# Kernel tuning notes

Measured on AMD Instinct MI355X. Metric: run time of the kernel, lower is better.

The kernel has to match this reference:

```python
import jax, jax.numpy as jnp
import numpy as np

B, C, H, W = 8, 384, 32, 32
NUM_HEADS = 8
HEAD_DIM = C // NUM_HEADS
HIDDEN = max(32, C // 2)


def setup_inputs() -> dict:
    key = jax.random.key(0)
    ks = jax.random.split(key, 6)
    s = lambda fan_in: 1.0 / np.sqrt(fan_in)
    return {
        "x": jax.random.normal(ks[0], (B, C, H, W), dtype=jnp.float32),
        "qkv_w": jax.random.normal(ks[1], (C, 3 * C), dtype=jnp.float32) * s(C),
        "qkv_b": jnp.zeros((3 * C,), dtype=jnp.float32),
        "proj_w": jax.random.normal(ks[2], (C, C), dtype=jnp.float32) * s(C),
        "proj_b": jnp.zeros((C,), dtype=jnp.float32),
        "mlp_w1": jax.random.normal(ks[3], (2, HIDDEN), dtype=jnp.float32) * s(2),
        "mlp_b1": jnp.zeros((HIDDEN,), dtype=jnp.float32),
        "mlp_w2": jax.random.normal(ks[4], (HIDDEN, NUM_HEADS), dtype=jnp.float32) * s(HIDDEN),
        "mlp_b2": jnp.zeros((NUM_HEADS,), dtype=jnp.float32),
    }


def _relative_bias(h, w, mlp_w1, mlp_b1, mlp_w2, mlp_b2):
    ch = jnp.arange(h, dtype=jnp.float32)
    cw = jnp.arange(w, dtype=jnp.float32)
    coords = jnp.stack(jnp.meshgrid(ch, cw, indexing="ij"), axis=-1).reshape(-1, 2)  # [N,2]
    rel = coords[:, None, :] - coords[None, :, :]  # [N,N,2]
    denom = jnp.array([max(h - 1, 1), max(w - 1, 1)], dtype=jnp.float32)
    rel = rel / denom
    hidden = jax.nn.gelu(rel @ mlp_w1 + mlp_b1, approximate=False)
    bias = hidden @ mlp_w2 + mlp_b2  # [N,N,heads]
    return jnp.transpose(bias, (2, 0, 1))  # [heads,N,N]


def reference(x, qkv_w, qkv_b, proj_w, proj_b, mlp_w1, mlp_b1, mlp_w2, mlp_b2):
    b, c, h, w = x.shape
    n = h * w
    tokens = x.reshape(b, c, n).transpose(0, 2, 1)  # [B,N,C]
    qkv = (tokens @ qkv_w + qkv_b).reshape(b, n, 3, NUM_HEADS, HEAD_DIM)
    qkv = jnp.transpose(qkv, (2, 0, 3, 1, 4))  # [3,B,h,N,d]
    q, k, v = qkv[0], qkv[1], qkv[2]
    scale = HEAD_DIM ** -0.5
    attn = jnp.einsum("bhnd,bhmd->bhnm", q * scale, k)
    attn = attn + _relative_bias(h, w, mlp_w1, mlp_b1, mlp_w2, mlp_b2)[None]
    attn = jax.nn.softmax(attn, axis=-1)
    out = jnp.einsum("bhnm,bhmd->bhnd", attn, v)
    out = out.transpose(0, 2, 1, 3).reshape(b, n, c)
    out = out @ proj_w + proj_b
    return out.transpose(0, 2, 1).reshape(b, c, h, w)
```

## Files before the change

kernel.cpp:

```cpp
#include <hip/hip_runtime.h>
#include <hip/hip_bf16.h>
#include <math.h>

#define BB 8
#define CC 384
#define NT 1024
#define NHEAD 8
#define HD 48
#define HIDDEN 192
#define THREEC 1152

typedef short short8 __attribute__((ext_vector_type(8)));
typedef short short4v __attribute__((ext_vector_type(4)));
typedef float f32x4 __attribute__((ext_vector_type(4)));
typedef unsigned int uint2v __attribute__((ext_vector_type(2)));
typedef unsigned int uint4v __attribute__((ext_vector_type(4)));

static __device__ __forceinline__ short bf16bits(float v) {
  __hip_bfloat16 h = __float2bfloat16(v);
  return *(short*)&h;
}
static __device__ __forceinline__ unsigned cvtpk(float lo, float hi) {
  unsigned r;
  asm("v_cvt_pk_bf16_f32 %0, %1, %2" : "=v"(r) : "v"(lo), "v"(hi));
  return r;
}
static __device__ __forceinline__ void lds_dma16(const void* g, void* l) {
  __builtin_amdgcn_global_load_lds((const __attribute__((address_space(1))) unsigned*)g,
                                   (__attribute__((address_space(3))) unsigned*)l, 16, 0, 0);
}
static __device__ __forceinline__ void pl16swap(unsigned& a, unsigned& b) {
  asm("v_permlane16_swap_b32 %0, %1" : "+v"(a), "+v"(b));
}
static __device__ __forceinline__ float exp2_raw(float x) {
  float r;
  asm("v_exp_f32 %0, %1" : "=v"(r) : "v"(x));
  return r;
}

__global__ __launch_bounds__(256) void k_prep(
    const float* __restrict__ x, const float* __restrict__ qkv_w,
    const float* __restrict__ proj_w,
    const float* __restrict__ w1, const float* __restrict__ b1,
    const float* __restrict__ w2, const float* __restrict__ b2,
    __hip_bfloat16* __restrict__ xt, __hip_bfloat16* __restrict__ wtq,
    __hip_bfloat16* __restrict__ wtp, float* __restrict__ tab) {
  const int bid = blockIdx.x;
  const int tid = threadIdx.x;
  if (bid >= 3648) {
    int g = (bid - 3648) * 256 + tid;
    int p = g >> 3, jc = g & 7;
    if (p >= 63 * 63) return;
    float rh = (float)(p / 63 - 31) * (1.0f / 31.0f);
    float rw = (float)(p % 63 - 31) * (1.0f / 31.0f);
    float acc[8] = {0.f, 0.f, 0.f, 0.f, 0.f, 0.f, 0.f, 0.f};
    const int j0 = jc * 24;
#pragma unroll 4
    for (int j = j0; j < j0 + 24; j++) {
      float pre = fmaf(rh, w1[j], fmaf(rw, w1[HIDDEN + j], b1[j]));
      float gl = 0.5f * pre * (1.0f + erff(pre * 0.70710678118654752f));
#pragma unroll
      for (int h = 0; h < 8; h++) acc[h] = fmaf(gl, w2[j * 8 + h], acc[h]);
    }
#pragma unroll
    for (int msk = 1; msk <= 4; msk <<= 1)
#pragma unroll
      for (int h = 0; h < 8; h++) acc[h] += __shfl_xor(acc[h], msk);
    if (jc == 0) {
#pragma unroll
      for (int h = 0; h < 8; h++)
        tab[h * 3969 + p] = (acc[h] + b2[h]) * 1.4426950408889634f;
    }
    return;
  }
  const float* src;
  __hip_bfloat16* dst;
  int R, C, r0, c0;
  if (bid < 3072) {
    int zi = bid / 384, rem = bid % 384;
    R = 384; C = 1024;
    r0 = (rem / 32) * 32; c0 = (rem % 32) * 32;
    src = x + (size_t)zi * R * C;
    dst = xt + (size_t)zi * R * C;
  } else if (bid < 3504) {
    int i = bid - 3072;
    R = 384; C = 1152;
    r0 = (i / 36) * 32; c0 = (i % 36) * 32;
    src = qkv_w; dst = wtq;
  } else {
    int i = bid - 3504;
    R = 384; C = 384;
    r0 = (i / 12) * 32; c0 = (i % 12) * 32;
    src = proj_w; dst = wtp;
  }
  __shared__ float t[32][33];
#pragma unroll
  for (int e = 0; e < 4; e++) {
    int i = tid + e * 256;
    int r = i >> 5, c = i & 31;
    t[r][c] = src[(size_t)(r0 + r) * C + c0 + c];
  }
  __syncthreads();
#pragma unroll
  for (int e = 0; e < 4; e++) {
    int i = tid + e * 256;
    int c = i >> 5, r = i & 31;
    dst[(size_t)(c0 + c) * R + r0 + r] = __float2bfloat16(t[r][c]);
  }
}

__global__ __launch_bounds__(256) void k_qkv_mfma(
    const __hip_bfloat16* __restrict__ xt,
    const __hip_bfloat16* __restrict__ wtq,
    const float* __restrict__ qkv_b,
    __hip_bfloat16* __restrict__ Qb,
    __hip_bfloat16* __restrict__ Kb,
    __hip_bfloat16* __restrict__ Vt)
{
  __shared__ __align__(16) char smem[17408];
  short* As = (short*)smem;
  short* Bs = (short*)(smem + 8192);
  float* Vf = (float*)smem;
  const int n0 = blockIdx.x * 64;
  const int m0 = blockIdx.y * 64;
  const int tid = threadIdx.x;
  const int wv = tid >> 6, lane = tid & 63, quad = lane >> 4, lq = lane & 15;
  const int lrow = lane >> 3;
  const int gsw = ((lane & 7) ^ lrow) * 8;
  const int sw0 = (quad ^ (lq & 7)) * 8;
  const int sw1 = sw0 ^ 32;
  f32x4 acc[4];
#pragma unroll
  for (int nt = 0; nt < 4; nt++) acc[nt] = (f32x4){0.f, 0.f, 0.f, 0.f};
  for (int kk = 0; kk < CC; kk += 64) {
    __syncthreads();
    for (int c = wv; c < 16; c += 4) {
      if (c < 8)
        lds_dma16((const short*)xt + (size_t)(m0 + c * 8 + lrow) * 384 + kk + gsw,
                  smem + c * 1024);
      else
        lds_dma16((const short*)wtq + (size_t)(n0 + (c - 8) * 8 + lrow) * 384 + kk + gsw,
                  smem + 8192 + (c - 8) * 1024);
    }
    __syncthreads();
    short8 a0 = *(const short8*)(As + (wv * 16 + lq) * 64 + sw0);
    short8 a1 = *(const short8*)(As + (wv * 16 + lq) * 64 + sw1);
#pragma unroll
    for (int nt = 0; nt < 4; nt++) {
      acc[nt] = __builtin_amdgcn_mfma_f32_16x16x32_bf16(
          a0, *(const short8*)(Bs + (nt * 16 + lq) * 64 + sw0), acc[nt], 0, 0, 0);
      acc[nt] = __builtin_amdgcn_mfma_f32_16x16x32_bf16(
          a1, *(const short8*)(Bs + (nt * 16 + lq) * 64 + sw1), acc[nt], 0, 0, 0);
    }
  }
  __syncthreads();
  const float qscale = 0.14433756729740643f * 1.4426950408889634f;
  const float sc = (n0 < 384) ? qscale : 1.0f;
#pragma unroll
  for (int nt = 0; nt < 4; nt++) {
    float bias = qkv_b[n0 + nt * 16 + lq];
#pragma unroll
    for (int r = 0; r < 4; r++)
      Vf[(nt * 16 + lq) * 68 + wv * 16 + quad * 4 + r] = (acc[nt][r] + bias) * sc;
  }
  __syncthreads();
  if (n0 >= 768) {
    int ch = tid & 63, grp = tid >> 6;
    int cg = n0 - 768 + ch;
    int head = cg / 48, d = cg - head * 48;
    int b = m0 >> 10;
    int n = (m0 & 1023) + grp * 16;
    const float* src = Vf + ch * 68 + grp * 16;
    short o16[16];
#pragma unroll
    for (int k = 0; k < 16; k++) o16[k] = bf16bits(src[k]);
    short* dst = (short*)Vt + ((size_t)(b * 8 + head) * 48 + d) * 1024 + n;
    *(short8*)dst = *(short8*)o16;
    *(short8*)(dst + 8) = *(short8*)(o16 + 8);
  } else {
    const int which = n0 >= 384;
    short* Out = which ? (short*)Kb : (short*)Qb;
    int n_l = tid & 63, seg = tid >> 6;
    int rr0 = (n0 - which * 384) + seg * 16;
    int head = rr0 / 48, d0 = rr0 - head * 48;
    int b = m0 >> 10;
    int n_g = (m0 & 1023) + n_l;
    const float* src = Vf + (seg * 16) * 68 + n_l;
    short o16[16];
#pragma unroll
    for (int k = 0; k < 16; k++) o16[k] = bf16bits(src[k * 68]);
    short* dst = Out + (((size_t)(b * 8 + head) << 10) + n_g) * 64 + d0;
    *(short8*)dst = *(short8*)o16;
    *(short8*)(dst + 8) = *(short8*)(o16 + 8);
    if (d0 == 0) {
      short8 z = (short8){0, 0, 0, 0, 0, 0, 0, 0};
      *(short8*)(dst + 48) = z;
      *(short8*)(dst + 56) = z;
    }
  }
}

#define K0_OFF 0
#define V0_OFF 16384
#define TR_OFF 28672
#define SMEM_SZ 32768
__global__ __launch_bounds__(256, 2) void k_flash(
    const __hip_bfloat16* __restrict__ Qb, const __hip_bfloat16* __restrict__ Kb,
    const __hip_bfloat16* __restrict__ Vt, const float* __restrict__ tab,
    __hip_bfloat16* __restrict__ ATb)
{
  __shared__ __align__(16) char smem[SMEM_SZ];
  float* Os = (float*)smem;

  const int tid = threadIdx.x;
  const int wv = tid >> 6, lane = tid & 63, quad = lane >> 4, lq = lane & 15;
  const int bh = blockIdx.x;
  const int q0 = blockIdx.y * 128;
  const int b = bh >> 3, h = bh & 7;
  const int inr0 = q0 >> 5;

  const int nrowA = q0 + wv * 32 + lq;
  const int tbaseA = (wv + 1) * 63 + lq + 31 - 4 * quad;
  const int tbaseB = tbaseA + 16;

  short8 qfA0, qfA1, qfB0, qfB1;
  {
    const short* qp = (const short*)Qb + ((size_t)(bh << 10) + nrowA) * 64;
    qfA0 = *(const short8*)(qp + quad * 8);
    qfA1 = *(const short8*)(qp + 32 + quad * 8);
    qfB0 = *(const short8*)(qp + 1024 + quad * 8);
    qfB1 = *(const short8*)(qp + 1024 + 32 + quad * 8);
  }
  short8 onesv;
#pragma unroll
  for (int j = 0; j < 8; j++) onesv[j] = (short)0x3F80;

  f32x4 OA[4], OB[4];
#pragma unroll
  for (int dt = 0; dt < 4; dt++) {
    OA[dt] = (f32x4){0.f, 0.f, 0.f, 0.f};
    OB[dt] = (f32x4){0.f, 0.f, 0.f, 0.f};
  }

  const short* kgp = (const short*)Kb + ((size_t)(bh << 10)) * 64;
  const short* vgp = (const short*)Vt + (size_t)bh * 48 * 1024;
  const float* tabg = tab + h * 3969;
  const int lrow = lane >> 3;
  const int gsw = ((lane & 7) ^ lrow) * 8;
  const int sw0 = (quad ^ (lq & 7)) * 8;
  const int sw1 = sw0 ^ 32;
  const int vq = ((quad & 1) << 1) | (quad >> 1);
  const int swv0 = (vq ^ (lq & 7)) * 8;
  const int swv1 = swv0 ^ 32;

  const char* kAsrc = (const char*)kgp + (((size_t)(wv * 8 + lrow) * 64 + gsw) << 1);
  const char* kBsrc = (const char*)kgp + (((size_t)((wv + 4) * 8 + lrow) * 64 + gsw) << 1);
  const int kAd = K0_OFF + wv * 1024;
  const int kBd = K0_OFF + (wv + 4) * 1024;
  const char* vsrc = (const char*)vgp + (((size_t)(wv * 8 + lrow) * 1024 + gsw) << 1);
  const int vd = V0_OFF + wv * 1024;
  const char* u4src;
  int u4stride, u4d, u4alt;
  if (wv < 2) {
    u4src = (const char*)vgp + (((size_t)((wv + 4) * 8 + lrow) * 1024 + gsw) << 1);
    u4stride = 128;
    u4d = V0_OFF + (wv + 4) * 1024;
    u4alt = 6144;
  } else {
    u4src = (const char*)(tabg + (inr0 + 30) * 63 + lane * 4 + (wv == 3 ? 256 : 0));
    u4stride = -504;
    u4d = TR_OFF + (wv == 3 ? 1024 : 0);
    u4alt = 2048;
  }
  lds_dma16(kAsrc, smem + kAd);
  lds_dma16(kBsrc, smem + kBd);
  lds_dma16(vsrc, smem + vd);
  lds_dma16(u4src, smem + u4d);

  for (int it = 0; it < 16; it++) {
    const int buf = it & 1;
    __syncthreads();
    if (it < 15) {
      const int nbuf = buf ^ 1;
      kAsrc += 8192; kBsrc += 8192; vsrc += 128; u4src += u4stride;
      lds_dma16(kAsrc, smem + kAd + nbuf * 8192);
      lds_dma16(kBsrc, smem + kBd + nbuf * 8192);
      lds_dma16(vsrc, smem + vd + nbuf * 6144);
      lds_dma16(u4src, smem + u4d + nbuf * u4alt);
    }
    const short* Kl = (const short*)(smem + K0_OFF + buf * 8192);
    const short* Vl = (const short*)(smem + V0_OFF + buf * 6144);
    const float* Tl = (const float*)(smem + TR_OFF + buf * 2048);

    float sA[4][4], sB[4][4];
    __builtin_amdgcn_s_setprio(1);
#pragma unroll
    for (int nt = 0; nt < 4; nt++) {
      short8 kf0 = *(const short8*)(Kl + (nt * 16 + lq) * 64 + sw0);
      short8 kf1 = *(const short8*)(Kl + (nt * 16 + lq) * 64 + sw1);
      const float* tnA = Tl + tbaseA - (nt >= 2 ? 63 : 0) - (nt & 1) * 16;
      f32x4 c;
      c[0] = tnA[0]; c[1] = tnA[-1]; c[2] = tnA[-2]; c[3] = tnA[-3];
      c = __builtin_amdgcn_mfma_f32_16x16x32_bf16(kf0, qfA0, c, 0, 0, 0);
      c = __builtin_amdgcn_mfma_f32_16x16x32_bf16(kf1, qfA1, c, 0, 0, 0);
#pragma unroll
      for (int r = 0; r < 4; r++) sA[nt][r] = c[r];
      const float* tnB = tnA + 16;
      f32x4 d;
      d[0] = tnB[0]; d[1] = tnB[-1]; d[2] = tnB[-2]; d[3] = tnB[-3];
      d = __builtin_amdgcn_mfma_f32_16x16x32_bf16(kf0, qfB0, d, 0, 0, 0);
      d = __builtin_amdgcn_mfma_f32_16x16x32_bf16(kf1, qfB1, d, 0, 0, 0);
#pragma unroll
      for (int r = 0; r < 4; r++) sB[nt][r] = d[r];
    }
    __builtin_amdgcn_s_setprio(0);
#pragma unroll
    for (int nt = 0; nt < 4; nt++)
#pragma unroll
      for (int r = 0; r < 4; r++) {
        sA[nt][r] = exp2_raw(sA[nt][r]);
        sB[nt][r] = exp2_raw(sB[nt][r]);
      }
    uint4v pA0, pA1, pB0, pB1;
    {
      unsigned a, bb_;
      a = cvtpk(sA[0][0], sA[0][1]); bb_ = cvtpk(sA[1][0], sA[1][1]);
      pl16swap(a, bb_); pA0[0] = a; pA0[2] = bb_;
      a = cvtpk(sA[0][2], sA[0][3]); bb_ = cvtpk(sA[1][2], sA[1][3]);
      pl16swap(a, bb_); pA0[1] = a; pA0[3] = bb_;
      a = cvtpk(sA[2][0], sA[2][1]); bb_ = cvtpk(sA[3][0], sA[3][1]);
      pl16swap(a, bb_); pA1[0] = a; pA1[2] = bb_;
      a = cvtpk(sA[2][2], sA[2][3]); bb_ = cvtpk(sA[3][2], sA[3][3]);
      pl16swap(a, bb_); pA1[1] = a; pA1[3] = bb_;
      a = cvtpk(sB[0][0], sB[0][1]); bb_ = cvtpk(sB[1][0], sB[1][1]);
      pl16swap(a, bb_); pB0[0] = a; pB0[2] = bb_;
      a = cvtpk(sB[0][2], sB[0][3]); bb_ = cvtpk(sB[1][2], sB[1][3]);
      pl16swap(a, bb_); pB0[1] = a; pB0[3] = bb_;
      a = cvtpk(sB[2][0], sB[2][1]); bb_ = cvtpk(sB[3][0], sB[3][1]);
      pl16swap(a, bb_); pB1[0] = a; pB1[2] = bb_;
      a = cvtpk(sB[2][2], sB[2][3]); bb_ = cvtpk(sB[3][2], sB[3][3]);
      pl16swap(a, bb_); pB1[1] = a; pB1[3] = bb_;
    }
    short8 pfA0 = *(short8*)&pA0;
    short8 pfA1 = *(short8*)&pA1;
    short8 pfB0 = *(short8*)&pB0;
    short8 pfB1 = *(short8*)&pB1;
    __builtin_amdgcn_s_setprio(1);
#pragma unroll
    for (int dt = 0; dt < 3; dt++) {
      short8 vf = *(const short8*)(Vl + (dt * 16 + lq) * 64 + swv0);
      OA[dt] = __builtin_amdgcn_mfma_f32_16x16x32_bf16(vf, pfA0, OA[dt], 0, 0, 0);
      OB[dt] = __builtin_amdgcn_mfma_f32_16x16x32_bf16(vf, pfB0, OB[dt], 0, 0, 0);
    }
    OA[3] = __builtin_amdgcn_mfma_f32_16x16x32_bf16(onesv, pfA0, OA[3], 0, 0, 0);
    OB[3] = __builtin_amdgcn_mfma_f32_16x16x32_bf16(onesv, pfB0, OB[3], 0, 0, 0);
#pragma unroll
    for (int dt = 0; dt < 3; dt++) {
      short8 vf = *(const short8*)(Vl + (dt * 16 + lq) * 64 + swv1);
      OA[dt] = __builtin_amdgcn_mfma_f32_16x16x32_bf16(vf, pfA1, OA[dt], 0, 0, 0);
      OB[dt] = __builtin_amdgcn_mfma_f32_16x16x32_bf16(vf, pfB1, OB[dt], 0, 0, 0);
    }
    OA[3] = __builtin_amdgcn_mfma_f32_16x16x32_bf16(onesv, pfA1, OA[3], 0, 0, 0);
    OB[3] = __builtin_amdgcn_mfma_f32_16x16x32_bf16(onesv, pfB1, OB[3], 0, 0, 0);
    __builtin_amdgcn_s_setprio(0);
  }
  float invA = 1.0f / OA[3][0];
  float invB = 1.0f / OB[3][0];
  __syncthreads();
#pragma unroll
  for (int dt = 0; dt < 3; dt++)
#pragma unroll
    for (int r = 0; r < 4; r++) {
      Os[(wv * 32 + lq) * 52 + dt * 16 + quad * 4 + r] = OA[dt][r] * invA;
      Os[(wv * 32 + 16 + lq) * 52 + dt * 16 + quad * 4 + r] = OB[dt][r] * invB;
    }
  __syncthreads();
  {
    int row = tid >> 1, cg = (tid & 1) * 24;
    const float* src = Os + row * 52 + cg;
    short outp[24];
#pragma unroll
    for (int k = 0; k < 24; k++) outp[k] = bf16bits(src[k]);
    short* dst = (short*)ATb + ((size_t)(b << 10) + q0 + row) * 384 + h * 48 + cg;
#pragma unroll
    for (int g = 0; g < 6; g++) *(short4v*)(dst + g * 4) = *(short4v*)(outp + g * 4);
  }
}

__global__ __launch_bounds__(256) void k_proj_mfma(
    const __hip_bfloat16* __restrict__ ATb,
    const __hip_bfloat16* __restrict__ wtp,
    const float* __restrict__ pb, float* __restrict__ out) {
  __shared__ __align__(16) char smem[16384];
  short* As = (short*)smem;
  short* Bs = (short*)(smem + 8192);
  const int c0 = blockIdx.x * 64;
  const int n0 = blockIdx.y * 64;
  const int b = blockIdx.z;
  const int tid = threadIdx.x;
  const int wv = tid >> 6, lane = tid & 63, quad = lane >> 4, lq = lane & 15;
  const int lrow = lane >> 3;
  const int gsw = ((lane & 7) ^ lrow) * 8;
  const int sw0 = (quad ^ (lq & 7)) * 8;
  const int sw1 = sw0 ^ 32;
  f32x4 acc[4];
#pragma unroll
  for (int nt = 0; nt < 4; nt++) acc[nt] = (f32x4){0.f, 0.f, 0.f, 0.f};
  for (int kk = 0; kk < CC; kk += 64) {
    __syncthreads();
    for (int c = wv; c < 16; c += 4) {
      if (c < 8)
        lds_dma16((const short*)wtp + (size_t)(c0 + c * 8 + lrow) * 384 + kk + gsw,
                  smem + c * 1024);
      else
        lds_dma16((const short*)ATb + ((size_t)(b << 10) + n0 + (c - 8) * 8 + lrow) * 384 + kk + gsw,
                  smem + 8192 + (c - 8) * 1024);
    }
    __syncthreads();
    short8 a0 = *(const short8*)(As + (wv * 16 + lq) * 64 + sw0);
    short8 a1 = *(const short8*)(As + (wv * 16 + lq) * 64 + sw1);
#pragma unroll
    for (int nt = 0; nt < 4; nt++) {
      acc[nt] = __builtin_amdgcn_mfma_f32_16x16x32_bf16(
          a0, *(const short8*)(Bs + (nt * 16 + lq) * 64 + sw0), acc[nt], 0, 0, 0);
      acc[nt] = __builtin_amdgcn_mfma_f32_16x16x32_bf16(
          a1, *(const short8*)(Bs + (nt * 16 + lq) * 64 + sw1), acc[nt], 0, 0, 0);
    }
  }
#pragma unroll
  for (int nt = 0; nt < 4; nt++) {
    int n = n0 + nt * 16 + lq;
#pragma unroll
    for (int r = 0; r < 4; r++) {
      int c = c0 + wv * 16 + quad * 4 + r;
      out[((size_t)b * 384 + c) * 1024 + n] = acc[nt][r] + pb[c];
    }
  }
}

extern "C" void kernel_launch(void* const* d_in, const int* in_sizes, int n_in,
                              void* d_out, int out_size, void* d_ws, size_t ws_size,
                              hipStream_t stream) {
  const float* x = (const float*)d_in[0];
  const float* qkv_w = (const float*)d_in[1];
  const float* qkv_b = (const float*)d_in[2];
  const float* proj_w = (const float*)d_in[3];
  const float* proj_b = (const float*)d_in[4];
  const float* w1 = (const float*)d_in[5];
  const float* b1 = (const float*)d_in[6];
  const float* w2 = (const float*)d_in[7];
  const float* b2 = (const float*)d_in[8];
  float* out = (float*)d_out;

  char* w = (char*)d_ws;
  __hip_bfloat16* xt = (__hip_bfloat16*)w;   w += (size_t)8192 * 384 * 2;
  __hip_bfloat16* wtq = (__hip_bfloat16*)w;  w += (size_t)1152 * 384 * 2;
  __hip_bfloat16* wtp = (__hip_bfloat16*)w;  w += (size_t)384 * 384 * 2;
  __hip_bfloat16* Qb = (__hip_bfloat16*)w;   w += (size_t)64 * 1024 * 64 * 2;
  __hip_bfloat16* Kb = (__hip_bfloat16*)w;   w += (size_t)64 * 1024 * 64 * 2;
  __hip_bfloat16* Vt = (__hip_bfloat16*)w;   w += (size_t)64 * 48 * 1024 * 2;
  __hip_bfloat16* ATb = (__hip_bfloat16*)w;  w += (size_t)8192 * 384 * 2;
  float* tab = (float*)w;                    w += (size_t)8 * 3969 * 4 + 1024;

  k_prep<<<dim3(3773), dim3(256), 0, stream>>>(x, qkv_w, proj_w, w1, b1, w2, b2,
                                               xt, wtq, wtp, tab);
  k_qkv_mfma<<<dim3(18, 128), dim3(256), 0, stream>>>(xt, wtq, qkv_b, Qb, Kb, Vt);
  k_flash<<<dim3(64, 8), dim3(256), 0, stream>>>(Qb, Kb, Vt, tab, ATb);
  k_proj_mfma<<<dim3(6, 16, 8), dim3(256), 0, stream>>>(ATb, wtp, proj_b, out);
}
```

Before: 151.0 us.

## Spread relative-bias MLP over more threads, stage weights in LDS, schedule first

The bias-table part of the prep kernel now uses 32 threads per relative offset instead of 8, each covering 6 hidden units rather than 24. The MLP weights are staged into shared memory, and the bias blocks are placed at the start of the grid instead of the end. The aim is to shorten the tail of the prep kernel, where a few long-running bias blocks were dispatched last behind thousands of transpose blocks. In exchange it launches more blocks, does longer shuffle reductions, and adds LDS staging with a barrier in every bias block.

```diff
diff --git a/kernel.cpp b/kernel.cpp
--- a/kernel.cpp
+++ b/kernel.cpp
@@ -38,6 +38,7 @@
   return r;
 }
 
+#define NB_BIAS 497
 __global__ __launch_bounds__(256) void k_prep(
     const float* __restrict__ x, const float* __restrict__ qkv_w,
     const float* __restrict__ proj_w,
@@ -47,23 +48,35 @@
     __hip_bfloat16* __restrict__ wtp, float* __restrict__ tab) {
   const int bid = blockIdx.x;
   const int tid = threadIdx.x;
-  if (bid >= 3648) {
-    int g = (bid - 3648) * 256 + tid;
-    int p = g >> 3, jc = g & 7;
+  if (bid < NB_BIAS) {
+    __shared__ float lw[2112];
+    for (int i = tid; i < 2112; i += 256) {
+      float v;
+      if (i < 384) v = w1[i];
+      else if (i < 576) v = b1[i - 384];
+      else v = w2[i - 576];
+      lw[i] = v;
+    }
+    __syncthreads();
+    const float* lw1 = lw;
+    const float* lb1 = lw + 384;
+    const float* lw2 = lw + 576;
+    int g = bid * 256 + tid;
+    int p = g >> 5, jc = g & 31;
     if (p >= 63 * 63) return;
     float rh = (float)(p / 63 - 31) * (1.0f / 31.0f);
     float rw = (float)(p % 63 - 31) * (1.0f / 31.0f);
     float acc[8] = {0.f, 0.f, 0.f, 0.f, 0.f, 0.f, 0.f, 0.f};
-    const int j0 = jc * 24;
-#pragma unroll 4
-    for (int j = j0; j < j0 + 24; j++) {
-      float pre = fmaf(rh, w1[j], fmaf(rw, w1[HIDDEN + j], b1[j]));
+    const int j0 = jc * 6;
+#pragma unroll
+    for (int j = j0; j < j0 + 6; j++) {
+      float pre = fmaf(rh, lw1[j], fmaf(rw, lw1[HIDDEN + j], lb1[j]));
       float gl = 0.5f * pre * (1.0f + erff(pre * 0.70710678118654752f));
 #pragma unroll
-      for (int h = 0; h < 8; h++) acc[h] = fmaf(gl, w2[j * 8 + h], acc[h]);
-    }
-#pragma unroll
-    for (int msk = 1; msk <= 4; msk <<= 1)
+      for (int h = 0; h < 8; h++) acc[h] = fmaf(gl, lw2[j * 8 + h], acc[h]);
+    }
+#pragma unroll
+    for (int msk = 1; msk <= 16; msk <<= 1)
 #pragma unroll
       for (int h = 0; h < 8; h++) acc[h] += __shfl_xor(acc[h], msk);
     if (jc == 0) {
@@ -73,22 +86,23 @@
     }
     return;
   }
+  const int tb = bid - NB_BIAS;
   const float* src;
   __hip_bfloat16* dst;
   int R, C, r0, c0;
-  if (bid < 3072) {
-    int zi = bid / 384, rem = bid % 384;
+  if (tb < 3072) {
+    int zi = tb / 384, rem = tb % 384;
     R = 384; C = 1024;
     r0 = (rem / 32) * 32; c0 = (rem % 32) * 32;
     src = x + (size_t)zi * R * C;
     dst = xt + (size_t)zi * R * C;
-  } else if (bid < 3504) {
-    int i = bid - 3072;
+  } else if (tb < 3504) {
+    int i = tb - 3072;
     R = 384; C = 1152;
     r0 = (i / 36) * 32; c0 = (i % 36) * 32;
     src = qkv_w; dst = wtq;
   } else {
-    int i = bid - 3504;
+    int i = tb - 3504;
     R = 384; C = 384;
     r0 = (i / 12) * 32; c0 = (i % 12) * 32;
     src = proj_w; dst = wtp;
@@ -462,7 +476,7 @@
   __hip_bfloat16* ATb = (__hip_bfloat16*)w;  w += (size_t)8192 * 384 * 2;
   float* tab = (float*)w;                    w += (size_t)8 * 3969 * 4 + 1024;
 
-  k_prep<<<dim3(3773), dim3(256), 0, stream>>>(x, qkv_w, proj_w, w1, b1, w2, b2,
+  k_prep<<<dim3(4145), dim3(256), 0, stream>>>(x, qkv_w, proj_w, w1, b1, w2, b2,
                                                xt, wtq, wtp, tab);
   k_qkv_mfma<<<dim3(18, 128), dim3(256), 0, stream>>>(xt, wtq, qkv_b, Qb, Kb, Vt);
   k_flash<<<dim3(64, 8), dim3(256), 0, stream>>>(Qb, Kb, Vt, tab, ATb);
```

Result: faster. 138.7 us (median of 2 runs) (-8.1%).
